# Kernel tuning notes

Measured on AMD Instinct MI355X. Metric: run time of the kernel, lower is better.

## Reference

```python
import jax, jax.numpy as jnp
import numpy as np

ROPE_BASE = 10000.0


def rotate_half(x):
    # interleaved rotate: (x0,x1,x2,x3,...) -> (-x1,x0,-x3,x2,...)
    x1 = x[..., ::2]
    x2 = x[..., 1::2]
    return jnp.stack((-x2, x1), axis=-1).reshape(x.shape)


def rope_cos_sin(seq_len, dim, dtype):
    inv_freq = 1.0 / (ROPE_BASE ** (jnp.arange(0, dim, 2, dtype=jnp.float32) / dim))
    pos = jnp.arange(seq_len, dtype=jnp.float32)
    freqs = jnp.outer(pos, inv_freq)              # [S, dim/2]
    emb = jnp.concatenate([freqs, freqs], axis=-1)  # [S, dim]
    return jnp.cos(emb).astype(dtype), jnp.sin(emb).astype(dtype)


def setup_inputs() -> dict:
    key = jax.random.key(0)
    k1, k2, k3, k4 = jax.random.split(key, 4)
    B, S, D = 4, 4096, 256
    scale = 1.0 / np.sqrt(D)
    x = jax.random.normal(k1, (B, S, D), dtype=jnp.float32)
    wq = jax.random.normal(k2, (D, D), dtype=jnp.float32) * scale
    wk = jax.random.normal(k3, (D, D), dtype=jnp.float32) * scale
    wv = jax.random.normal(k4, (D, D), dtype=jnp.float32) * scale
    return {"x": x, "wq": wq, "wk": wk, "wv": wv}


def reference(x, wq, wk, wv):
    D = x.shape[-1]
    S = x.shape[-2]
    # torch Linear: y = x @ W^T
    q = jnp.einsum('bsd,ed->bse', x, wq)
    k = jnp.einsum('bsd,ed->bse', x, wk)
    v = jnp.einsum('bsd,ed->bse', x, wv)
    cos, sin = rope_cos_sin(S, D, x.dtype)  # [S, D]
    q = q * cos + rotate_half(q) * sin
    k = k * cos + rotate_half(k) * sin
    scores = jnp.einsum('bqd,bkd->bqk', q, k) / jnp.sqrt(jnp.asarray(D, x.dtype))
    weights = jax.nn.softmax(scores, axis=-1)
    output = jnp.einsum('bqk,bkd->bqd', weights, v)
    return output, weights
```

## Files before the change

kernel.cpp:

```cpp
#include <hip/hip_runtime.h>
#include <hip/hip_bf16.h>
#include <stdint.h>


#define B_ 4
#define S_ 4096
#define D_ 256
#define NQ 4194304
#define NW 65536
#define NTAB 524288

typedef __attribute__((ext_vector_type(4))) float f32x4;
typedef __attribute__((ext_vector_type(8))) short short8;
typedef __attribute__((ext_vector_type(4))) short short4v;
typedef __attribute__((ext_vector_type(4))) unsigned uint32x4;

__device__ __forceinline__ short f2bf(float f) {
  unsigned u = __builtin_bit_cast(unsigned, f);
  u += 0x7fffu + ((u >> 16) & 1u);
  return (short)(u >> 16);
}
__device__ __forceinline__ float bf2f(short h) {
  unsigned u = ((unsigned)(unsigned short)h) << 16;
  return __builtin_bit_cast(float, u);
}

__device__ __forceinline__ void gload16(const void* g, void* l) {
  __builtin_amdgcn_global_load_lds(
      (const __attribute__((address_space(1))) unsigned*)g,
      (__attribute__((address_space(3))) unsigned*)l, 16, 0, 0);
}

__global__ __launch_bounds__(256) void k0_split(
    const float* __restrict__ x, const float* __restrict__ wq,
    const float* __restrict__ wk, const float* __restrict__ wv,
    short* __restrict__ xh, short* __restrict__ xl,
    short* __restrict__ wh, short* __restrict__ wl,
    float* __restrict__ ctab) {
  int idx = blockIdx.x * 256 + threadIdx.x;
  if (idx < NQ) {
    float v = x[idx];
    short hi = f2bf(v);
    xh[idx] = hi;
    xl[idx] = f2bf(v - bf2f(hi));
  } else if (idx < NQ + 3 * NW) {
    int r = idx - NQ;
    int m = r >> 16;
    int e = r & (NW - 1);
    const float* w = (m == 0) ? wq : (m == 1) ? wk : wv;
    float v = w[e];
    short hi = f2bf(v);
    wh[r] = hi;
    wl[r] = f2bf(v - bf2f(hi));
  } else {
    int t = idx - NQ - 3 * NW;
    int s = t >> 7, j = t & 127;
    float invf = __expf(-0.07195578415606394f * (float)j);
    float sn, cs;
    sincosf((float)s * invf, &sn, &cs);
    ctab[2 * t] = cs;
    ctab[2 * t + 1] = sn;
  }
}

__global__ __launch_bounds__(256) void k1_proj(
    const short* __restrict__ xh, const short* __restrict__ xl,
    const short* __restrict__ wh, const short* __restrict__ wl,
    const float* __restrict__ ctab,
    short* __restrict__ qh, short* __restrict__ ql,
    short* __restrict__ kh, short* __restrict__ kl,
    short* __restrict__ vt) {
  const int m = blockIdx.y;
  const int b = blockIdx.x >> 6;
  const int sbase = (blockIdx.x & 63) << 6;
  const int tid = threadIdx.x;
  const int w = tid >> 6;
  const int lane = tid & 63;
  const int lr = lane & 15;
  const int g = lane >> 4;

  const int srow = sbase + w * 16 + lr;
  const short* xhp = xh + ((size_t)(b * S_ + srow)) * D_;
  const short* xlp = xl + ((size_t)(b * S_ + srow)) * D_;
  const short* whm = wh + m * NW;
  const short* wlm = wl + m * NW;

  f32x4 acc[16];
#pragma unroll
  for (int i = 0; i < 16; ++i) acc[i] = (f32x4)0.f;

#pragma unroll
  for (int dc = 0; dc < 8; ++dc) {
    const int d = dc * 32 + g * 8;
    short8 ah = *(const short8*)(xhp + d);
    short8 al = *(const short8*)(xlp + d);
#pragma unroll
    for (int ct = 0; ct < 16; ++ct) {
      const int e = ct * 16 + lr;
      short8 bh = *(const short8*)(whm + e * D_ + d);
      short8 bl = *(const short8*)(wlm + e * D_ + d);
      acc[ct] = __builtin_amdgcn_mfma_f32_16x16x32_bf16(ah, bh, acc[ct], 0, 0, 0);
      acc[ct] = __builtin_amdgcn_mfma_f32_16x16x32_bf16(ah, bl, acc[ct], 0, 0, 0);
      acc[ct] = __builtin_amdgcn_mfma_f32_16x16x32_bf16(al, bh, acc[ct], 0, 0, 0);
    }
  }

  const int s0 = sbase + w * 16 + g * 4;
  if (m == 2) {
#pragma unroll
    for (int ct = 0; ct < 16; ++ct) {
      const int e = ct * 16 + lr;
      short4v pk;
#pragma unroll
      for (int r = 0; r < 4; ++r) pk[r] = f2bf(acc[ct][r]);
      *(short4v*)(vt + ((size_t)(b * D_ + e)) * S_ + s0) = pk;
    }
  } else {
    short* oh = (m == 0) ? qh : kh;
    short* ol = (m == 0) ? ql : kl;
#pragma unroll
    for (int ct = 0; ct < 16; ++ct) {
      const int e = ct * 16 + lr;
      const float sgn = (e & 1) ? 1.0f : -1.0f;
#pragma unroll
      for (int r = 0; r < 4; ++r) {
        float v = acc[ct][r];
        float p = __shfl_xor(v, 1, 64);
        const float2 cs2 = *(const float2*)(ctab + ((size_t)((s0 + r) << 7) + (e & 127)) * 2);
        float q2 = v * cs2.x + sgn * p * cs2.y;
        short hi = f2bf(q2);
        size_t off = ((size_t)(b * S_ + s0 + r)) * D_ + e;
        oh[off] = hi;
        ol[off] = f2bf(q2 - bf2f(hi));
      }
    }
  }
}

__global__ __launch_bounds__(512, 2) void k2_fused(
    const short* __restrict__ qh, const short* __restrict__ ql,
    const short* __restrict__ kh, const short* __restrict__ kl,
    const short* __restrict__ vt,
    float* __restrict__ wts, float* __restrict__ out) {
  __shared__ __align__(16) char sbuf[65536];
  __shared__ __align__(16) char etile[8192];
  __shared__ float part[4][64];
  __shared__ float lsum_l[64];

  const int bid = blockIdx.x;
  const int swz = (bid & 7) * 32 + (bid >> 3);
  const int b = swz >> 6;
  const int qbase = (swz & 63) << 6;
  const int tid = threadIdx.x;
  const int w = tid >> 6;
  const int lane = tid & 63;
  const int lr = lane & 15;
  const int g = lane >> 4;
  const int wq2 = w & 1;
  const int wk4 = w >> 1;
  const int qh_pv = w & 1;
  const int dh_pv = w >> 1;

  short8 qfh[2][8], qfl[2][8];
#pragma unroll
  for (int qt = 0; qt < 2; ++qt) {
    const int qrow = qbase + wq2 * 32 + qt * 16 + lr;
    const short* ph = qh + ((size_t)(b * S_ + qrow)) * D_;
    const short* pl = ql + ((size_t)(b * S_ + qrow)) * D_;
#pragma unroll
    for (int dc = 0; dc < 8; ++dc) {
      qfh[qt][dc] = *(const short8*)(ph + dc * 32 + g * 8);
      qfl[qt][dc] = *(const short8*)(pl + dc * 32 + g * 8);
    }
  }

  f32x4 acc[2];
  acc[0] = (f32x4)0.f; acc[1] = (f32x4)0.f;
  f32x4 accv[2][4];
#pragma unroll
  for (int qt = 0; qt < 2; ++qt)
#pragma unroll
    for (int dt = 0; dt < 4; ++dt) accv[qt][dt] = (f32x4)0.f;
  float rs[2] = {0.f, 0.f};

  const char* khb = (const char*)(kh + (size_t)b * S_ * D_);
  const char* klb = (const char*)(kl + (size_t)b * S_ * D_);
  const short* vtb = vt + (size_t)b * D_ * S_;
  const int keyl = wk4 * 16 + lr;
  const int swx = (lane & 7) << 4;

  char* WB = (char*)(wts + ((size_t)(b * S_ + qbase)) * S_);
  char* EB = WB + 524288;

  {
#pragma unroll
    for (int i = 0; i < 4; ++i) {
      const int p = i * 8192 + tid * 16;
      const int xo = p ^ (((p >> 9) & 7) << 4);
      gload16(khb + xo, sbuf + p);
      gload16(klb + xo, sbuf + 32768 + p);
    }
  }
  __syncthreads();

  for (int kt = 0; kt < 64; ++kt) {
#pragma unroll
    for (int dc = 0; dc < 8; ++dc) {
      const int x = (keyl * 512 + dc * 64 + g * 16) ^ swx;
      short8 afh = *(const short8*)(sbuf + x);
      short8 afl = *(const short8*)(sbuf + 32768 + x);
      acc[0] = __builtin_amdgcn_mfma_f32_16x16x32_bf16(afh, qfh[0][dc], acc[0], 0, 0, 0);
      acc[0] = __builtin_amdgcn_mfma_f32_16x16x32_bf16(afh, qfl[0][dc], acc[0], 0, 0, 0);
      acc[0] = __builtin_amdgcn_mfma_f32_16x16x32_bf16(afl, qfh[0][dc], acc[0], 0, 0, 0);
      acc[1] = __builtin_amdgcn_mfma_f32_16x16x32_bf16(afh, qfh[1][dc], acc[1], 0, 0, 0);
      acc[1] = __builtin_amdgcn_mfma_f32_16x16x32_bf16(afh, qfl[1][dc], acc[1], 0, 0, 0);
      acc[1] = __builtin_amdgcn_mfma_f32_16x16x32_bf16(afl, qfh[1][dc], acc[1], 0, 0, 0);
    }

#pragma unroll
    for (int qt = 0; qt < 2; ++qt) {
      f32x4 e;
#pragma unroll
      for (int r = 0; r < 4; ++r) e[r] = __expf(acc[qt][r] * 0.0625f);
      rs[qt] += e[0] + e[1] + e[2] + e[3];
      unsigned lo = (unsigned)(unsigned short)f2bf(e[0]) |
                    ((unsigned)(unsigned short)f2bf(e[1]) << 16);
      unsigned hi2 = (unsigned)(unsigned short)f2bf(e[2]) |
                     ((unsigned)(unsigned short)f2bf(e[3]) << 16);
      const int row = wq2 * 32 + qt * 16 + lr;
      const int colb = (wk4 * 16 + g * 4) * 2;
      const int ad = (row * 128 + colb) ^ ((row & 7) << 4);
      *(uint2*)(etile + ad) = make_uint2(lo, hi2);
      acc[qt] = (f32x4)0.f;
    }
    __syncthreads();

    if (kt < 63) {
      const char* sh = khb + (size_t)(kt + 1) * 64 * D_ * 2;
      const char* sl = klb + (size_t)(kt + 1) * 64 * D_ * 2;
#pragma unroll
      for (int i = 0; i < 4; ++i) {
        const int p = i * 8192 + tid * 16;
        const int xo = p ^ (((p >> 9) & 7) << 4);
        gload16(sh + xo, sbuf + p);
        gload16(sl + xo, sbuf + 32768 + p);
      }
    }

    {
      const int p = tid * 16;
      const int row = p >> 7, cb = p & 127;
      uint32x4 v = *(const uint32x4*)(etile + (p ^ ((row & 7) << 4)));
      *(uint32x4*)(EB + (size_t)row * 8192 + kt * 128 + cb) = v;
    }

#pragma unroll
    for (int kk = 0; kk < 2; ++kk) {
      short8 ea0, ea1;
      {
        const int row = qh_pv * 32 + lr;
        ea0 = *(const short8*)(etile + ((row * 128 + kk * 64 + g * 16) ^ ((row & 7) << 4)));
      }
      {
        const int row = qh_pv * 32 + 16 + lr;
        ea1 = *(const short8*)(etile + ((row * 128 + kk * 64 + g * 16) ^ ((row & 7) << 4)));
      }
#pragma unroll
      for (int dt = 0; dt < 4; ++dt) {
        const int d = dh_pv * 64 + dt * 16 + lr;
        short8 vb = *(const short8*)(vtb + (size_t)d * S_ + kt * 64 + kk * 32 + g * 8);
        accv[0][dt] = __builtin_amdgcn_mfma_f32_16x16x32_bf16(ea0, vb, accv[0][dt], 0, 0, 0);
        accv[1][dt] = __builtin_amdgcn_mfma_f32_16x16x32_bf16(ea1, vb, accv[1][dt], 0, 0, 0);
      }
    }
    __syncthreads();
  }

#pragma unroll
  for (int qt = 0; qt < 2; ++qt) {
    rs[qt] += __shfl_xor(rs[qt], 16, 64);
    rs[qt] += __shfl_xor(rs[qt], 32, 64);
  }
  if (lane < 16) {
    part[wk4][wq2 * 32 + lane] = rs[0];
    part[wk4][wq2 * 32 + 16 + lane] = rs[1];
  }
  __syncthreads();
  if (tid < 64)
    lsum_l[tid] = part[0][tid] + part[1][tid] + part[2][tid] + part[3][tid];
  __syncthreads();

#pragma unroll
  for (int i = 0; i < 2; ++i) {
    const int p = i * 8192 + tid * 16;
    *(uint32x4*)(sbuf + p) = *(const uint32x4*)(EB + (size_t)62 * 8192 + p);
  }

  {
    float* ob = out + (size_t)b * S_ * D_;
    float rv[2][4];
#pragma unroll
    for (int qt = 0; qt < 2; ++qt)
#pragma unroll
      for (int r = 0; r < 4; ++r)
        rv[qt][r] = 1.0f / lsum_l[qh_pv * 32 + qt * 16 + g * 4 + r];
#pragma unroll
    for (int qt = 0; qt < 2; ++qt)
#pragma unroll
      for (int dt = 0; dt < 4; ++dt)
#pragma unroll
        for (int r = 0; r < 4; ++r) {
          const int q = qbase + qh_pv * 32 + qt * 16 + g * 4 + r;
          ob[(size_t)q * D_ + dh_pv * 64 + dt * 16 + lr] = accv[qt][dt][r] * rv[qt][r];
        }
  }
  __syncthreads();

  const int pr0[6] = {0, 32, 48, 56, 60, 62};
  const int pr1[6] = {32, 48, 56, 60, 62, 64};
#pragma unroll 1
  for (int ph = 0; ph < 6; ++ph) {
    for (int r = pr0[ph] + w; r < pr1[ph]; r += 8) {
      const float rinv = 1.0f / lsum_l[r];
      const short* erow = (r >= 62) ? (const short*)(sbuf + (size_t)(r - 62) * 8192)
                                    : (const short*)(EB + (size_t)r * 8192);
      float* wrow = (float*)(WB + (size_t)r * 16384);
      for (int c = lane * 8; c < 4096; c += 512) {
        short8 ev = *(const short8*)(erow + c);
        f32x4 o0, o1;
#pragma unroll
        for (int j = 0; j < 4; ++j) o0[j] = bf2f(ev[j]) * rinv;
#pragma unroll
        for (int j = 0; j < 4; ++j) o1[j] = bf2f(ev[4 + j]) * rinv;
        *(f32x4*)(wrow + c) = o0;
        *(f32x4*)(wrow + c + 4) = o1;
      }
    }
    __syncthreads();
  }
}

extern "C" void kernel_launch(void* const* d_in, const int* in_sizes, int n_in,
                              void* d_out, int out_size, void* d_ws, size_t ws_size,
                              hipStream_t stream) {
  const float* x  = (const float*)d_in[0];
  const float* wq = (const float*)d_in[1];
  const float* wk = (const float*)d_in[2];
  const float* wv = (const float*)d_in[3];

  float* out = (float*)d_out;
  float* wts = out + (size_t)B_ * S_ * D_;

  short* xh = (short*)d_ws;
  short* xl = xh + NQ;
  short* qh = xl + NQ;
  short* ql = qh + NQ;
  short* kh = ql + NQ;
  short* kl = kh + NQ;
  short* vt = kl + NQ;
  short* wh = vt + NQ;
  short* wl = wh + 3 * NW;
  float* ctab = (float*)(wl + 3 * NW);

  k0_split<<<dim3((NQ + 3 * NW + NTAB) / 256), 256, 0, stream>>>(
      x, wq, wk, wv, xh, xl, wh, wl, ctab);
  k1_proj<<<dim3(B_ * S_ / 64, 3), 256, 0, stream>>>(
      xh, xl, wh, wl, ctab, qh, ql, kh, kl, vt);
  k2_fused<<<dim3(B_ * S_ / 64), 512, 0, stream>>>(
      qh, ql, kh, kl, vt, wts, out);
}
```

Measured before the change: 486.6 us.

## Double-buffer K tiles and software-pipeline PV with the next QK tile

K hi/lo tiles are now double-buffered in LDS. The next tile's prefetch is issued at the start of each iteration, and the P·V MFMAs for the previous tile are interleaved with the QK MFMAs of the current tile using a double-buffered exp tile. This cuts the synchronisation to one barrier per iteration, and s_setprio raises priority around the MFMA sections. The cost is a much larger LDS footprint: about 145KB per block against the earlier ~75KB. That likely drops residency from 2 blocks to 1 per CU despite the launch bounds.

```diff
diff --git a/kernel.cpp b/kernel.cpp
--- a/kernel.cpp
+++ b/kernel.cpp
@@ -142,8 +142,8 @@
     const short* __restrict__ kh, const short* __restrict__ kl,
     const short* __restrict__ vt,
     float* __restrict__ wts, float* __restrict__ out) {
-  __shared__ __align__(16) char sbuf[65536];
-  __shared__ __align__(16) char etile[8192];
+  __shared__ __align__(16) char kbuf[131072];
+  __shared__ __align__(16) char etile[2][8192];
   __shared__ float part[4][64];
   __shared__ float lsum_l[64];
 
@@ -192,23 +192,69 @@
   char* WB = (char*)(wts + ((size_t)(b * S_ + qbase)) * S_);
   char* EB = WB + 524288;
 
-  {
-#pragma unroll
-    for (int i = 0; i < 4; ++i) {
-      const int p = i * 8192 + tid * 16;
-      const int xo = p ^ (((p >> 9) & 7) << 4);
-      gload16(khb + xo, sbuf + p);
-      gload16(klb + xo, sbuf + 32768 + p);
-    }
+#pragma unroll
+  for (int i = 0; i < 4; ++i) {
+    const int p = i * 8192 + tid * 16;
+    const int xo = p ^ (((p >> 9) & 7) << 4);
+    gload16(khb + xo, kbuf + p);
+    gload16(klb + xo, kbuf + 32768 + p);
   }
   __syncthreads();
 
   for (int kt = 0; kt < 64; ++kt) {
+    const int cur = kt & 1;
+    const char* kb = kbuf + cur * 65536;
+
+    if (kt < 63) {
+      const char* sh = khb + (size_t)(kt + 1) * 32768;
+      const char* sl = klb + (size_t)(kt + 1) * 32768;
+      char* kn = kbuf + (cur ^ 1) * 65536;
+#pragma unroll
+      for (int i = 0; i < 4; ++i) {
+        const int p = i * 8192 + tid * 16;
+        const int xo = p ^ (((p >> 9) & 7) << 4);
+        gload16(sh + xo, kn + p);
+        gload16(sl + xo, kn + 32768 + p);
+      }
+    }
+
+    if (kt > 0) {
+      const char* et = etile[cur ^ 1];
+      {
+        const int p = tid * 16;
+        const int row = p >> 7, cb = p & 127;
+        uint32x4 v = *(const uint32x4*)(et + (p ^ ((row & 7) << 4)));
+        *(uint32x4*)(EB + (size_t)row * 8192 + (kt - 1) * 128 + cb) = v;
+      }
+      __builtin_amdgcn_s_setprio(1);
+#pragma unroll
+      for (int kk = 0; kk < 2; ++kk) {
+        short8 ea0, ea1;
+        {
+          const int row = qh_pv * 32 + lr;
+          ea0 = *(const short8*)(et + ((row * 128 + kk * 64 + g * 16) ^ ((row & 7) << 4)));
+        }
+        {
+          const int row = qh_pv * 32 + 16 + lr;
+          ea1 = *(const short8*)(et + ((row * 128 + kk * 64 + g * 16) ^ ((row & 7) << 4)));
+        }
+#pragma unroll
+        for (int dt = 0; dt < 4; ++dt) {
+          const int d = dh_pv * 64 + dt * 16 + lr;
+          short8 vb = *(const short8*)(vtb + (size_t)d * S_ + (kt - 1) * 64 + kk * 32 + g * 8);
+          accv[0][dt] = __builtin_amdgcn_mfma_f32_16x16x32_bf16(ea0, vb, accv[0][dt], 0, 0, 0);
+          accv[1][dt] = __builtin_amdgcn_mfma_f32_16x16x32_bf16(ea1, vb, accv[1][dt], 0, 0, 0);
+        }
+      }
+      __builtin_amdgcn_s_setprio(0);
+    }
+
+    __builtin_amdgcn_s_setprio(1);
 #pragma unroll
     for (int dc = 0; dc < 8; ++dc) {
       const int x = (keyl * 512 + dc * 64 + g * 16) ^ swx;
-      short8 afh = *(const short8*)(sbuf + x);
-      short8 afl = *(const short8*)(sbuf + 32768 + x);
+      short8 afh = *(const short8*)(kb + x);
+      short8 afl = *(const short8*)(kb + 32768 + x);
       acc[0] = __builtin_amdgcn_mfma_f32_16x16x32_bf16(afh, qfh[0][dc], acc[0], 0, 0, 0);
       acc[0] = __builtin_amdgcn_mfma_f32_16x16x32_bf16(afh, qfl[0][dc], acc[0], 0, 0, 0);
       acc[0] = __builtin_amdgcn_mfma_f32_16x16x32_bf16(afl, qfh[0][dc], acc[0], 0, 0, 0);
@@ -216,6 +262,7 @@
       acc[1] = __builtin_amdgcn_mfma_f32_16x16x32_bf16(afh, qfl[1][dc], acc[1], 0, 0, 0);
       acc[1] = __builtin_amdgcn_mfma_f32_16x16x32_bf16(afl, qfh[1][dc], acc[1], 0, 0, 0);
     }
+    __builtin_amdgcn_s_setprio(0);
 
 #pragma unroll
     for (int qt = 0; qt < 2; ++qt) {
@@ -230,50 +277,39 @@
       const int row = wq2 * 32 + qt * 16 + lr;
       const int colb = (wk4 * 16 + g * 4) * 2;
       const int ad = (row * 128 + colb) ^ ((row & 7) << 4);
-      *(uint2*)(etile + ad) = make_uint2(lo, hi2);
+      *(uint2*)(etile[cur] + ad) = make_uint2(lo, hi2);
       acc[qt] = (f32x4)0.f;
     }
     __syncthreads();
-
-    if (kt < 63) {
-      const char* sh = khb + (size_t)(kt + 1) * 64 * D_ * 2;
-      const char* sl = klb + (size_t)(kt + 1) * 64 * D_ * 2;
-#pragma unroll
-      for (int i = 0; i < 4; ++i) {
-        const int p = i * 8192 + tid * 16;
-        const int xo = p ^ (((p >> 9) & 7) << 4);
-        gload16(sh + xo, sbuf + p);
-        gload16(sl + xo, sbuf + 32768 + p);
-      }
-    }
-
+  }
+
+  {
+    const char* et = etile[1];
     {
       const int p = tid * 16;
       const int row = p >> 7, cb = p & 127;
-      uint32x4 v = *(const uint32x4*)(etile + (p ^ ((row & 7) << 4)));
-      *(uint32x4*)(EB + (size_t)row * 8192 + kt * 128 + cb) = v;
-    }
-
+      uint32x4 v = *(const uint32x4*)(et + (p ^ ((row & 7) << 4)));
+      *(uint32x4*)(EB + (size_t)row * 8192 + 63 * 128 + cb) = v;
+    }
 #pragma unroll
     for (int kk = 0; kk < 2; ++kk) {
       short8 ea0, ea1;
       {
         const int row = qh_pv * 32 + lr;
-        ea0 = *(const short8*)(etile + ((row * 128 + kk * 64 + g * 16) ^ ((row & 7) << 4)));
+        ea0 = *(const short8*)(et + ((row * 128 + kk * 64 + g * 16) ^ ((row & 7) << 4)));
       }
       {
         const int row = qh_pv * 32 + 16 + lr;
-        ea1 = *(const short8*)(etile + ((row * 128 + kk * 64 + g * 16) ^ ((row & 7) << 4)));
+        ea1 = *(const short8*)(et + ((row * 128 + kk * 64 + g * 16) ^ ((row & 7) << 4)));
       }
 #pragma unroll
       for (int dt = 0; dt < 4; ++dt) {
         const int d = dh_pv * 64 + dt * 16 + lr;
-        short8 vb = *(const short8*)(vtb + (size_t)d * S_ + kt * 64 + kk * 32 + g * 8);
+        short8 vb = *(const short8*)(vtb + (size_t)d * S_ + 63 * 64 + kk * 32 + g * 8);
         accv[0][dt] = __builtin_amdgcn_mfma_f32_16x16x32_bf16(ea0, vb, accv[0][dt], 0, 0, 0);
         accv[1][dt] = __builtin_amdgcn_mfma_f32_16x16x32_bf16(ea1, vb, accv[1][dt], 0, 0, 0);
       }
     }
-    __syncthreads();
   }
 
 #pragma unroll
@@ -293,7 +329,7 @@
 #pragma unroll
   for (int i = 0; i < 2; ++i) {
     const int p = i * 8192 + tid * 16;
-    *(uint32x4*)(sbuf + p) = *(const uint32x4*)(EB + (size_t)62 * 8192 + p);
+    *(uint32x4*)(kbuf + p) = *(const uint32x4*)(EB + (size_t)62 * 8192 + p);
   }
 
   {
@@ -322,7 +358,7 @@
   for (int ph = 0; ph < 6; ++ph) {
     for (int r = pr0[ph] + w; r < pr1[ph]; r += 8) {
       const float rinv = 1.0f / lsum_l[r];
-      const short* erow = (r >= 62) ? (const short*)(sbuf + (size_t)(r - 62) * 8192)
+      const short* erow = (r >= 62) ? (const short*)(kbuf + (size_t)(r - 62) * 8192)
                                     : (const short*)(EB + (size_t)r * 8192);
       float* wrow = (float*)(WB + (size_t)r * 16384);
       for (int c = lane * 8; c < 4096; c += 512) {
```

Measured after the change: 473.6 us. -2.7%, faster.

## Double-buffer K tiles with manual waitcnt pipelining and stage projection stores via LDS

Applied to the files above, without the earlier changes.

The fused attention kernel now double-buffers the K hi/lo tiles in 128KB of LDS, prefetching two tiles ahead and replacing full __syncthreads with explicit vmcnt waits and s_barrier. V fragments are loaded at the top of each iteration, and the MFMA sections run under raised s_setprio. Occupancy drops to one block per CU to fit the larger LDS footprint. The projection kernel now stages the RoPE'd q/k hi/lo outputs through shared memory so they can be written with coalesced 16-byte stores instead of scattered 2-byte writes.

```diff
diff --git a/kernel.cpp b/kernel.cpp
--- a/kernel.cpp
+++ b/kernel.cpp
@@ -70,6 +70,7 @@
     short* __restrict__ qh, short* __restrict__ ql,
     short* __restrict__ kh, short* __restrict__ kl,
     short* __restrict__ vt) {
+  __shared__ short tbuf[16384];
   const int m = blockIdx.y;
   const int b = blockIdx.x >> 6;
   const int sbase = (blockIdx.x & 63) << 6;
@@ -127,23 +128,46 @@
         float v = acc[ct][r];
         float p = __shfl_xor(v, 1, 64);
         const float2 cs2 = *(const float2*)(ctab + ((size_t)((s0 + r) << 7) + (e & 127)) * 2);
-        float q2 = v * cs2.x + sgn * p * cs2.y;
-        short hi = f2bf(q2);
-        size_t off = ((size_t)(b * S_ + s0 + r)) * D_ + e;
-        oh[off] = hi;
-        ol[off] = f2bf(q2 - bf2f(hi));
-      }
-    }
-  }
-}
-
-__global__ __launch_bounds__(512, 2) void k2_fused(
+        acc[ct][r] = v * cs2.x + sgn * p * cs2.y;
+      }
+    }
+    const int rowb = w * 16 + g * 4;
+    const size_t gbase = ((size_t)(b * S_ + sbase)) * D_;
+#pragma unroll
+    for (int ct = 0; ct < 16; ++ct)
+#pragma unroll
+      for (int r = 0; r < 4; ++r)
+        tbuf[(rowb + r) * 256 + ct * 16 + lr] = f2bf(acc[ct][r]);
+    __syncthreads();
+#pragma unroll
+    for (int j = 0; j < 8; ++j) {
+      const int L = j * 2048 + tid * 8;
+      *(short8*)(oh + gbase + L) = *(const short8*)(tbuf + L);
+    }
+    __syncthreads();
+#pragma unroll
+    for (int ct = 0; ct < 16; ++ct)
+#pragma unroll
+      for (int r = 0; r < 4; ++r) {
+        float q2 = acc[ct][r];
+        tbuf[(rowb + r) * 256 + ct * 16 + lr] = f2bf(q2 - bf2f(f2bf(q2)));
+      }
+    __syncthreads();
+#pragma unroll
+    for (int j = 0; j < 8; ++j) {
+      const int L = j * 2048 + tid * 8;
+      *(short8*)(ol + gbase + L) = *(const short8*)(tbuf + L);
+    }
+  }
+}
+
+__global__ __launch_bounds__(512, 1) void k2_fused(
     const short* __restrict__ qh, const short* __restrict__ ql,
     const short* __restrict__ kh, const short* __restrict__ kl,
     const short* __restrict__ vt,
     float* __restrict__ wts, float* __restrict__ out) {
-  __shared__ __align__(16) char sbuf[65536];
-  __shared__ __align__(16) char etile[8192];
+  __shared__ __align__(16) char kbuf[131072];
+  __shared__ __align__(16) char etile[2][8192];
   __shared__ float part[4][64];
   __shared__ float lsum_l[64];
 
@@ -192,23 +216,43 @@
   char* WB = (char*)(wts + ((size_t)(b * S_ + qbase)) * S_);
   char* EB = WB + 524288;
 
-  {
+  auto STAGE = [&](int kt, char* dst) {
 #pragma unroll
     for (int i = 0; i < 4; ++i) {
       const int p = i * 8192 + tid * 16;
       const int xo = p ^ (((p >> 9) & 7) << 4);
-      gload16(khb + xo, sbuf + p);
-      gload16(klb + xo, sbuf + 32768 + p);
-    }
-  }
-  __syncthreads();
+      gload16(khb + (size_t)kt * 32768 + xo, dst + p);
+      gload16(klb + (size_t)kt * 32768 + xo, dst + 32768 + p);
+    }
+  };
+
+  STAGE(0, kbuf);
+  STAGE(1, kbuf + 65536);
 
   for (int kt = 0; kt < 64; ++kt) {
+    const int cur = kt & 1;
+    const char* kb = kbuf + cur * 65536;
+
+    if (kt == 0)      asm volatile("s_waitcnt vmcnt(8)" ::: "memory");
+    else if (kt == 1) asm volatile("s_waitcnt vmcnt(17)" ::: "memory");
+    else if (kt < 63) asm volatile("s_waitcnt vmcnt(18)" ::: "memory");
+    else              asm volatile("s_waitcnt vmcnt(10)" ::: "memory");
+    __builtin_amdgcn_s_barrier();
+    __builtin_amdgcn_sched_barrier(0);
+
+    short8 vb[2][4];
+#pragma unroll
+    for (int kk = 0; kk < 2; ++kk)
+#pragma unroll
+      for (int dt = 0; dt < 4; ++dt)
+        vb[kk][dt] = *(const short8*)(vtb + (size_t)(dh_pv * 64 + dt * 16 + lr) * S_ + kt * 64 + kk * 32 + g * 8);
+
+    __builtin_amdgcn_s_setprio(1);
 #pragma unroll
     for (int dc = 0; dc < 8; ++dc) {
       const int x = (keyl * 512 + dc * 64 + g * 16) ^ swx;
-      short8 afh = *(const short8*)(sbuf + x);
-      short8 afl = *(const short8*)(sbuf + 32768 + x);
+      short8 afh = *(const short8*)(kb + x);
+      short8 afl = *(const short8*)(kb + 32768 + x);
       acc[0] = __builtin_amdgcn_mfma_f32_16x16x32_bf16(afh, qfh[0][dc], acc[0], 0, 0, 0);
       acc[0] = __builtin_amdgcn_mfma_f32_16x16x32_bf16(afh, qfl[0][dc], acc[0], 0, 0, 0);
       acc[0] = __builtin_amdgcn_mfma_f32_16x16x32_bf16(afl, qfh[0][dc], acc[0], 0, 0, 0);
@@ -216,6 +260,7 @@
       acc[1] = __builtin_amdgcn_mfma_f32_16x16x32_bf16(afh, qfl[1][dc], acc[1], 0, 0, 0);
       acc[1] = __builtin_amdgcn_mfma_f32_16x16x32_bf16(afl, qfh[1][dc], acc[1], 0, 0, 0);
     }
+    __builtin_amdgcn_s_setprio(0);
 
 #pragma unroll
     for (int qt = 0; qt < 2; ++qt) {
@@ -230,50 +275,43 @@
       const int row = wq2 * 32 + qt * 16 + lr;
       const int colb = (wk4 * 16 + g * 4) * 2;
       const int ad = (row * 128 + colb) ^ ((row & 7) << 4);
-      *(uint2*)(etile + ad) = make_uint2(lo, hi2);
+      *(uint2*)(etile[cur] + ad) = make_uint2(lo, hi2);
       acc[qt] = (f32x4)0.f;
     }
-    __syncthreads();
-
-    if (kt < 63) {
-      const char* sh = khb + (size_t)(kt + 1) * 64 * D_ * 2;
-      const char* sl = klb + (size_t)(kt + 1) * 64 * D_ * 2;
-#pragma unroll
-      for (int i = 0; i < 4; ++i) {
-        const int p = i * 8192 + tid * 16;
-        const int xo = p ^ (((p >> 9) & 7) << 4);
-        gload16(sh + xo, sbuf + p);
-        gload16(sl + xo, sbuf + 32768 + p);
-      }
-    }
+
+    asm volatile("s_waitcnt lgkmcnt(0)" ::: "memory");
+    __builtin_amdgcn_s_barrier();
+    __builtin_amdgcn_sched_barrier(0);
+
+    if (kt < 62) STAGE(kt + 2, kbuf + cur * 65536);
 
     {
+      const char* et = etile[cur];
       const int p = tid * 16;
       const int row = p >> 7, cb = p & 127;
-      uint32x4 v = *(const uint32x4*)(etile + (p ^ ((row & 7) << 4)));
+      uint32x4 v = *(const uint32x4*)(et + (p ^ ((row & 7) << 4)));
       *(uint32x4*)(EB + (size_t)row * 8192 + kt * 128 + cb) = v;
     }
 
+    __builtin_amdgcn_s_setprio(1);
 #pragma unroll
     for (int kk = 0; kk < 2; ++kk) {
       short8 ea0, ea1;
       {
         const int row = qh_pv * 32 + lr;
-        ea0 = *(const short8*)(etile + ((row * 128 + kk * 64 + g * 16) ^ ((row & 7) << 4)));
+        ea0 = *(const short8*)(etile[cur] + ((row * 128 + kk * 64 + g * 16) ^ ((row & 7) << 4)));
       }
       {
         const int row = qh_pv * 32 + 16 + lr;
-        ea1 = *(const short8*)(etile + ((row * 128 + kk * 64 + g * 16) ^ ((row & 7) << 4)));
+        ea1 = *(const short8*)(etile[cur] + ((row * 128 + kk * 64 + g * 16) ^ ((row & 7) << 4)));
       }
 #pragma unroll
       for (int dt = 0; dt < 4; ++dt) {
-        const int d = dh_pv * 64 + dt * 16 + lr;
-        short8 vb = *(const short8*)(vtb + (size_t)d * S_ + kt * 64 + kk * 32 + g * 8);
-        accv[0][dt] = __builtin_amdgcn_mfma_f32_16x16x32_bf16(ea0, vb, accv[0][dt], 0, 0, 0);
-        accv[1][dt] = __builtin_amdgcn_mfma_f32_16x16x32_bf16(ea1, vb, accv[1][dt], 0, 0, 0);
-      }
-    }
-    __syncthreads();
+        accv[0][dt] = __builtin_amdgcn_mfma_f32_16x16x32_bf16(ea0, vb[kk][dt], accv[0][dt], 0, 0, 0);
+        accv[1][dt] = __builtin_amdgcn_mfma_f32_16x16x32_bf16(ea1, vb[kk][dt], accv[1][dt], 0, 0, 0);
+      }
+    }
+    __builtin_amdgcn_s_setprio(0);
   }
 
 #pragma unroll
@@ -293,7 +331,7 @@
 #pragma unroll
   for (int i = 0; i < 2; ++i) {
     const int p = i * 8192 + tid * 16;
-    *(uint32x4*)(sbuf + p) = *(const uint32x4*)(EB + (size_t)62 * 8192 + p);
+    *(uint32x4*)(kbuf + p) = *(const uint32x4*)(EB + (size_t)62 * 8192 + p);
   }
 
   {
@@ -318,13 +356,14 @@
 
   const int pr0[6] = {0, 32, 48, 56, 60, 62};
   const int pr1[6] = {32, 48, 56, 60, 62, 64};
+  float* WBf = (float*)WB;
 #pragma unroll 1
   for (int ph = 0; ph < 6; ++ph) {
     for (int r = pr0[ph] + w; r < pr1[ph]; r += 8) {
       const float rinv = 1.0f / lsum_l[r];
-      const short* erow = (r >= 62) ? (const short*)(sbuf + (size_t)(r - 62) * 8192)
+      const short* erow = (r >= 62) ? (const short*)(kbuf + (size_t)(r - 62) * 8192)
                                     : (const short*)(EB + (size_t)r * 8192);
-      float* wrow = (float*)(WB + (size_t)r * 16384);
+      float* wrow = WBf + (size_t)r * 4096;
       for (int c = lane * 8; c < 4096; c += 512) {
         short8 ev = *(const short8*)(erow + c);
         f32x4 o0, o1;
```

Measured after the change: 513.9 us. +5.6%, slower.
